# Optimization experiments

Hardware: AMD Instinct MI355X
Metric: run time of the kernel (lower is better)

The kernel has to match this reference:

```python
import math
import jax, jax.numpy as jnp
import numpy as np

N, T, C, C2, H, W = 4, 8, 256, 256, 32, 32


def setup_inputs() -> dict:
    key = jax.random.key(0)
    k1, k2, k3 = jax.random.split(key, 3)
    return {
        "key": jax.random.normal(k1, (N, T, C, H, W), dtype=jnp.float32),
        "query": jax.random.normal(k2, (N, T, C, H, W), dtype=jnp.float32),
        "value": jax.random.normal(k3, (N, T, C2, H, W), dtype=jnp.float32),
    }


def reference(key, query, value):
    n, t, c, h, w = key.shape
    c2 = value.shape[2]
    hw = h * w
    k = key.reshape(n, t, c, hw)      # (n,t,c,p)
    q = query.reshape(n, t, c, hw)    # (n,t,c,q)
    v = value.reshape(n, t, c2, hw)   # (n,t,c2,p)
    # scores[p,q] = sum_c K[c,p] * Q[c,q], scaled by sqrt(c)
    scores = jnp.einsum("ntcp,ntcq->ntpq", k, q) / math.sqrt(c)
    # non-standard: softmax over the KEY axis (dim=-2)
    p_attn = jax.nn.softmax(scores, axis=-2)
    # non-standard: V @ attn (contract over key positions p)
    p_val = jnp.einsum("ntcp,ntpq->ntcq", v, p_attn).reshape(n, t, c2, h, w)
    return p_val, p_attn.reshape(n, t, h, w, h, w)
```

## Files before the change

### kernel.cpp

```cpp
#include <hip/hip_runtime.h>
#include <hip/hip_bf16.h>


#define NT_BATCH 32
#define CDIM     256
#define HW       1024

using short8 = __attribute__((ext_vector_type(8))) short;
using f32x16 = __attribute__((ext_vector_type(16))) float;
using f32x4v = __attribute__((ext_vector_type(4))) float;

__device__ __forceinline__ unsigned pk2(float a, float b) {
  float2 t; t.x = a; t.y = b;
  __hip_bfloat162 h = __float22bfloat162_rn(t);
  return *reinterpret_cast<unsigned*>(&h);
}
__device__ __forceinline__ void wr64(void* dst, float a, float b, float c, float d) {
  uint2 v; v.x = pk2(a, b); v.y = pk2(c, d);
  *reinterpret_cast<uint2*>(dst) = v;
}

union SMEM {
  struct { unsigned short Qs[64][264]; unsigned short As[256][72]; } a;
  struct { unsigned short Vs[256][72]; unsigned short Ps[64][72]; } b;
};

__global__ __launch_bounds__(512, 4) void k_fused(const float* __restrict__ Kp,
                                                  const float* __restrict__ Qp,
                                                  const float* __restrict__ Vp,
                                                  float* __restrict__ A_out,
                                                  float* __restrict__ O) {
  __shared__ __align__(16) SMEM sm;
  __shared__ float csum[64];
  __shared__ float inv_s[64];

  const int hbid = blockIdx.y * 16 + blockIdx.x;
  const int lbid = ((hbid & 7) << 6) | (hbid >> 3);
  const int nt = lbid >> 4;
  const int q0 = (lbid & 15) << 6;

  const float* Kb = Kp + (size_t)nt * (CDIM * HW);
  const float* Qb = Qp + (size_t)nt * (CDIM * HW);
  const float* Vb = Vp + (size_t)nt * (CDIM * HW);
  float* Ab = A_out + (size_t)nt * (HW * HW);
  float* Ob = O + (size_t)nt * (CDIM * HW);

  const int t = threadIdx.x, lane = t & 63;
  const int wave = t >> 6;
  const int l31 = lane & 31, lhi = lane >> 5;

  if (t < 64) csum[t] = 0.f;

  #pragma unroll
  for (int j2 = 0; j2 < 2; ++j2) {
    const int u = t + (j2 << 9);
    const int cb4 = (u & 63) << 2, qb4 = (u >> 6) << 2;
    f32x4v qv[4];
    #pragma unroll
    for (int j = 0; j < 4; ++j)
      qv[j] = *(const f32x4v*)&Qb[(size_t)(cb4 + j) * HW + q0 + qb4];
    #pragma unroll
    for (int i = 0; i < 4; ++i)
      wr64(&sm.a.Qs[qb4 + i][cb4], qv[0][i], qv[1][i], qv[2][i], qv[3][i]);
  }

  f32x4v kreg[2][4];
  auto loadK = [&](int P0_, int C0_) {
    #pragma unroll
    for (int j2 = 0; j2 < 2; ++j2) {
      const int u = t + (j2 << 9);
      const int cb = (u & 15) << 2, pp = (u >> 4) << 2;
      #pragma unroll
      for (int j = 0; j < 4; ++j)
        kreg[j2][j] = *(const f32x4v*)&Kb[(size_t)(C0_ + cb + j) * HW + P0_ + pp];
    }
  };

  float part[2] = {0.f, 0.f};
  loadK(0, 0);
  for (int pt = 0; pt < 4; ++pt) {
    const int P0 = pt << 8;
    f32x16 acc[2];
    #pragma unroll
    for (int n = 0; n < 2; ++n)
      #pragma unroll
      for (int r = 0; r < 16; ++r) acc[n][r] = 0.f;

    #pragma unroll
    for (int cc = 0; cc < 4; ++cc) {
      __syncthreads();
      #pragma unroll
      for (int j2 = 0; j2 < 2; ++j2) {
        const int u = t + (j2 << 9);
        const int cb = (u & 15) << 2, pp = (u >> 4) << 2;
        #pragma unroll
        for (int i = 0; i < 4; ++i)
          wr64(&sm.a.As[pp + i][cb],
               kreg[j2][0][i], kreg[j2][1][i], kreg[j2][2][i], kreg[j2][3][i]);
      }
      if (cc < 3) loadK(P0, (cc + 1) << 6);
      else if (pt < 3) loadK(P0 + 256, 0);
      __syncthreads();
      #pragma unroll
      for (int ks = 0; ks < 4; ++ks) {
        short8 a_ = *(const short8*)&sm.a.As[wave * 32 + l31][ks * 16 + lhi * 8];
        short8 b0 = *(const short8*)&sm.a.Qs[l31][(cc << 6) + ks * 16 + lhi * 8];
        short8 b1 = *(const short8*)&sm.a.Qs[32 + l31][(cc << 6) + ks * 16 + lhi * 8];
        acc[0] = __builtin_amdgcn_mfma_f32_32x32x16_bf16(a_, b0, acc[0], 0, 0, 0);
        acc[1] = __builtin_amdgcn_mfma_f32_32x32x16_bf16(a_, b1, acc[1], 0, 0, 0);
      }
    }

    const int rbase = wave * 32 + (lhi << 2);
    #pragma unroll
    for (int n = 0; n < 2; ++n) {
      const int col = q0 + n * 32 + l31;
      #pragma unroll
      for (int r = 0; r < 16; ++r) {
        float e = __expf(acc[n][r] * 0.0625f);
        part[n] += e;
        const int row = P0 + rbase + (r & 3) + ((r >> 2) << 3);
        Ab[(size_t)row * HW + col] = e;
      }
    }
  }

  atomicAdd(&csum[l31], part[0]);
  atomicAdd(&csum[32 + l31], part[1]);
  __syncthreads();
  if (t < 64) inv_s[t] = 1.0f / csum[t];
  __syncthreads();

  const int pr2 = t >> 4;
  const int sq = (t & 15) << 2;
  const f32x4v inv4 = *(const f32x4v*)&inv_s[sq];
  const int vc = t >> 1, vp = (t & 1) << 5;

  f32x4v er[2];
  f32x4v vreg[8];
  auto loadE = [&](int pb_) {
    er[0] = *(const f32x4v*)&Ab[(size_t)(pb_ + 2 * pr2) * HW + q0 + sq];
    er[1] = *(const f32x4v*)&Ab[(size_t)(pb_ + 2 * pr2 + 1) * HW + q0 + sq];
  };
  auto loadV = [&](int pb_) {
    #pragma unroll
    for (int g = 0; g < 8; ++g)
      vreg[g] = *(const f32x4v*)&Vb[(size_t)vc * HW + pb_ + vp + (g << 2)];
  };

  f32x16 av[2];
  #pragma unroll
  for (int n = 0; n < 2; ++n)
    #pragma unroll
    for (int r = 0; r < 16; ++r) av[n][r] = 0.f;

  loadE(0); loadV(0);
  for (int tile = 0; tile < 16; ++tile) {
    const int pb = tile << 6;
    const f32x4v a0 = er[0] * inv4;
    const f32x4v a1 = er[1] * inv4;
    __syncthreads();
    #pragma unroll
    for (int j = 0; j < 4; ++j)
      *reinterpret_cast<unsigned*>(&sm.b.Ps[sq + j][2 * pr2]) = pk2(a0[j], a1[j]);
    #pragma unroll
    for (int g = 0; g < 4; ++g) {
      uint4 w_;
      w_.x = pk2(vreg[2 * g][0], vreg[2 * g][1]);
      w_.y = pk2(vreg[2 * g][2], vreg[2 * g][3]);
      w_.z = pk2(vreg[2 * g + 1][0], vreg[2 * g + 1][1]);
      w_.w = pk2(vreg[2 * g + 1][2], vreg[2 * g + 1][3]);
      *reinterpret_cast<uint4*>(&sm.b.Vs[vc][vp + (g << 3)]) = w_;
    }
    if (tile < 15) { loadE(pb + 64); loadV(pb + 64); }
    *(f32x4v*)&Ab[(size_t)(pb + 2 * pr2) * HW + q0 + sq] = a0;
    *(f32x4v*)&Ab[(size_t)(pb + 2 * pr2 + 1) * HW + q0 + sq] = a1;
    __syncthreads();
    #pragma unroll
    for (int kk = 0; kk < 4; ++kk) {
      short8 a_ = *(const short8*)&sm.b.Vs[wave * 32 + l31][kk * 16 + lhi * 8];
      short8 b0 = *(const short8*)&sm.b.Ps[l31][kk * 16 + lhi * 8];
      short8 b1 = *(const short8*)&sm.b.Ps[32 + l31][kk * 16 + lhi * 8];
      av[0] = __builtin_amdgcn_mfma_f32_32x32x16_bf16(a_, b0, av[0], 0, 0, 0);
      av[1] = __builtin_amdgcn_mfma_f32_32x32x16_bf16(a_, b1, av[1], 0, 0, 0);
    }
  }

  #pragma unroll
  for (int n = 0; n < 2; ++n) {
    const int col = q0 + n * 32 + l31;
    const int cbase = wave * 32 + (lhi << 2);
    #pragma unroll
    for (int r = 0; r < 16; ++r) {
      const int c = cbase + (r & 3) + ((r >> 2) << 3);
      Ob[(size_t)c * HW + col] = av[n][r];
    }
  }
}

extern "C" void kernel_launch(void* const* d_in, const int* in_sizes, int n_in,
                              void* d_out, int out_size, void* d_ws, size_t ws_size,
                              hipStream_t stream) {
  const float* key   = (const float*)d_in[0];
  const float* query = (const float*)d_in[1];
  const float* value = (const float*)d_in[2];
  float* out  = (float*)d_out;
  float* pval = out;
  float* attn = out + (size_t)NT_BATCH * CDIM * HW;

  k_fused<<<dim3(16, NT_BATCH), 512, 0, stream>>>(key, query, value, attn, pval);
}
```

Baseline: 420.4 us.

## Replace syncthreads with LDS-only barriers, unroll loops, double-buffer E prefetch

Replaces __syncthreads with a barrier that waits only on LDS counters (lgkmcnt), so in-flight global prefetches of K, V and E are not drained at every barrier. Raises wave priority around the MFMA loops and fully unrolls the outer pt and tile loops. Double-buffers the exp-score reload two tiles ahead to deepen the prefetch. The risks are higher register pressure from unrolling and the extra E buffer, which could hurt occupancy at launch_bounds(512,4). The E reload also still reads back attention rows that this thread block wrote itself, which depends on memory ordering.

```diff
diff --git a/kernel.cpp b/kernel.cpp
--- a/kernel.cpp
+++ b/kernel.cpp
@@ -18,6 +18,13 @@
 __device__ __forceinline__ void wr64(void* dst, float a, float b, float c, float d) {
   uint2 v; v.x = pk2(a, b); v.y = pk2(c, d);
   *reinterpret_cast<uint2*>(dst) = v;
+}
+
+__device__ __forceinline__ void barrier_lgkm() {
+  __builtin_amdgcn_sched_barrier(0);
+  asm volatile("s_waitcnt lgkmcnt(0)" ::: "memory");
+  __builtin_amdgcn_s_barrier();
+  __builtin_amdgcn_sched_barrier(0);
 }
 
 union SMEM {
@@ -78,6 +85,7 @@
 
   float part[2] = {0.f, 0.f};
   loadK(0, 0);
+  #pragma unroll
   for (int pt = 0; pt < 4; ++pt) {
     const int P0 = pt << 8;
     f32x16 acc[2];
@@ -88,7 +96,7 @@
 
     #pragma unroll
     for (int cc = 0; cc < 4; ++cc) {
-      __syncthreads();
+      barrier_lgkm();
       #pragma unroll
       for (int j2 = 0; j2 < 2; ++j2) {
         const int u = t + (j2 << 9);
@@ -100,7 +108,8 @@
       }
       if (cc < 3) loadK(P0, (cc + 1) << 6);
       else if (pt < 3) loadK(P0 + 256, 0);
-      __syncthreads();
+      barrier_lgkm();
+      __builtin_amdgcn_s_setprio(1);
       #pragma unroll
       for (int ks = 0; ks < 4; ++ks) {
         short8 a_ = *(const short8*)&sm.a.As[wave * 32 + l31][ks * 16 + lhi * 8];
@@ -109,6 +118,7 @@
         acc[0] = __builtin_amdgcn_mfma_f32_32x32x16_bf16(a_, b0, acc[0], 0, 0, 0);
         acc[1] = __builtin_amdgcn_mfma_f32_32x32x16_bf16(a_, b1, acc[1], 0, 0, 0);
       }
+      __builtin_amdgcn_s_setprio(0);
     }
 
     const int rbase = wave * 32 + (lhi << 2);
@@ -136,11 +146,11 @@
   const f32x4v inv4 = *(const f32x4v*)&inv_s[sq];
   const int vc = t >> 1, vp = (t & 1) << 5;
 
-  f32x4v er[2];
+  f32x4v er[2][2];
   f32x4v vreg[8];
-  auto loadE = [&](int pb_) {
-    er[0] = *(const f32x4v*)&Ab[(size_t)(pb_ + 2 * pr2) * HW + q0 + sq];
-    er[1] = *(const f32x4v*)&Ab[(size_t)(pb_ + 2 * pr2 + 1) * HW + q0 + sq];
+  auto loadE = [&](int buf, int pb_) {
+    er[buf][0] = *(const f32x4v*)&Ab[(size_t)(pb_ + 2 * pr2) * HW + q0 + sq];
+    er[buf][1] = *(const f32x4v*)&Ab[(size_t)(pb_ + 2 * pr2 + 1) * HW + q0 + sq];
   };
   auto loadV = [&](int pb_) {
     #pragma unroll
@@ -154,12 +164,14 @@
     #pragma unroll
     for (int r = 0; r < 16; ++r) av[n][r] = 0.f;
 
-  loadE(0); loadV(0);
+  loadE(0, 0); loadV(0); loadE(1, 64);
+  #pragma unroll
   for (int tile = 0; tile < 16; ++tile) {
     const int pb = tile << 6;
-    const f32x4v a0 = er[0] * inv4;
-    const f32x4v a1 = er[1] * inv4;
-    __syncthreads();
+    const int cur = tile & 1;
+    const f32x4v a0 = er[cur][0] * inv4;
+    const f32x4v a1 = er[cur][1] * inv4;
+    barrier_lgkm();
     #pragma unroll
     for (int j = 0; j < 4; ++j)
       *reinterpret_cast<unsigned*>(&sm.b.Ps[sq + j][2 * pr2]) = pk2(a0[j], a1[j]);
@@ -172,10 +184,12 @@
       w_.w = pk2(vreg[2 * g + 1][2], vreg[2 * g + 1][3]);
       *reinterpret_cast<uint4*>(&sm.b.Vs[vc][vp + (g << 3)]) = w_;
     }
-    if (tile < 15) { loadE(pb + 64); loadV(pb + 64); }
+    if (tile < 15) loadV(pb + 64);
+    if (tile < 14) loadE(cur, pb + 128);
     *(f32x4v*)&Ab[(size_t)(pb + 2 * pr2) * HW + q0 + sq] = a0;
     *(f32x4v*)&Ab[(size_t)(pb + 2 * pr2 + 1) * HW + q0 + sq] = a1;
-    __syncthreads();
+    barrier_lgkm();
+    __builtin_amdgcn_s_setprio(1);
     #pragma unroll
     for (int kk = 0; kk < 4; ++kk) {
       short8 a_ = *(const short8*)&sm.b.Vs[wave * 32 + l31][kk * 16 + lhi * 8];
@@ -184,6 +198,7 @@
       av[0] = __builtin_amdgcn_mfma_f32_32x32x16_bf16(a_, b0, av[0], 0, 0, 0);
       av[1] = __builtin_amdgcn_mfma_f32_32x32x16_bf16(a_, b1, av[1], 0, 0, 0);
     }
+    __builtin_amdgcn_s_setprio(0);
   }
 
   #pragma unroll
```

Result: faster. 406.9 us (-3.2%).
